# Performance work log

Measured on AMD Instinct MI355X. Metric: run time of the kernel, lower is better.

Reference implementation:

```python
import jax, jax.numpy as jnp
import numpy as np

N = 4096  # output_size
B = 4096  # batch rows
NEG_SLOPE = 0.02


def setup_inputs() -> dict:
    key = jax.random.key(0)
    k1, k2, k3, k4 = jax.random.split(key, 4)
    x = jax.random.normal(k1, (B, N), dtype=jnp.float32)
    W = jax.random.normal(k2, (N, N), dtype=jnp.float32)        # self.weights
    beta = jax.random.normal(k3, (1,), dtype=jnp.float32)       # self.beta (scalar param)
    beta_res = jax.random.normal(k4, (N,), dtype=jnp.float32)   # self.res.beta
    return {"x": x, "W": W, "beta": beta, "beta_res": beta_res}


def reference(x, W, beta, beta_res):
    # wrho = x.unsqueeze(1) * W.expand(B,-1,-1); row_sum = wrho.sum(2)  ==  x @ W.T
    row_sum = jnp.einsum("bj,ij->bi", x, W)                 # [B, N]
    out = jax.nn.relu(1.0 - beta + row_sum)                 # hlogic(1 - beta + row_sum)
    # ResEventually: relu(1 - (beta_res - (x + out))), then LeakyReLU(0.02)
    res = jax.nn.relu(1.0 - (beta_res - (x + out)))
    return jnp.where(res >= 0, res, NEG_SLOPE * res)
```

## Files before the change

### kernel.cpp

```cpp
#include <hip/hip_runtime.h>


#define NDIM 4096

typedef __bf16 bf16x8 __attribute__((ext_vector_type(8)));
typedef float f32x4 __attribute__((ext_vector_type(4)));

__device__ unsigned short f2bf(float f) {
    unsigned int x;
    __builtin_memcpy(&x, &f, 4);
    unsigned int r = x + 0x7FFFu + ((x >> 16) & 1u);
    return (unsigned short)(r >> 16);
}

__device__ unsigned int pack_bf2(float lo, float hi) {
    return (unsigned int)f2bf(lo) | ((unsigned int)f2bf(hi) << 16);
}

__device__ inline void gload16(const uint4* g, unsigned int* l) {
    __builtin_amdgcn_global_load_lds(
        (const __attribute__((address_space(1))) unsigned int*)g,
        (__attribute__((address_space(3))) unsigned int*)l,
        16, 0, 0);
}

__global__ void convert_f32_bf16_kernel(const float* X, unsigned int* Xbf,
                                        const float* W, unsigned int* Wbf) {
    unsigned int bid = blockIdx.x;
    const float* src;
    unsigned int* dst;
    if (bid < 4096) { src = X; dst = Xbf; }
    else            { src = W; dst = Wbf; bid -= 4096; }
    const size_t i = ((size_t)bid * blockDim.x + threadIdx.x) * 16;
    const f32x4* s4 = (const f32x4*)(src + i);
    f32x4 a = __builtin_nontemporal_load(s4);
    f32x4 b = __builtin_nontemporal_load(s4 + 1);
    f32x4 c = __builtin_nontemporal_load(s4 + 2);
    f32x4 d = __builtin_nontemporal_load(s4 + 3);
    uint4 u0, u1;
    u0.x = pack_bf2(a[0], a[1]);  u0.y = pack_bf2(a[2], a[3]);
    u0.z = pack_bf2(b[0], b[1]);  u0.w = pack_bf2(b[2], b[3]);
    u1.x = pack_bf2(c[0], c[1]);  u1.y = pack_bf2(c[2], c[3]);
    u1.z = pack_bf2(d[0], d[1]);  u1.w = pack_bf2(d[2], d[3]);
    uint4* o4 = (uint4*)(dst + i / 2);
    o4[0] = u0;
    o4[1] = u1;
}

#define BAR()   __builtin_amdgcn_s_barrier()
#define VMCNT(n) asm volatile("s_waitcnt vmcnt(" #n ")" ::: "memory")
#define PRIO(x) __builtin_amdgcn_s_setprio(x)

#define STAGE_A(buf, h, S) do { \
    gload16(Ab4 + (offA[2*(h)]   + (S)*8), &sAU[buf][(2*(h))*2048   + wq]); \
    gload16(Ab4 + (offA[2*(h)+1] + (S)*8), &sAU[buf][(2*(h)+1)*2048 + wq]); \
} while (0)
#define STAGE_B(buf, h, S) do { \
    gload16(Bb4 + (offB[2*(h)]   + (S)*8), &sBU[buf][(2*(h))*2048   + wq]); \
    gload16(Bb4 + (offB[2*(h)+1] + (S)*8), &sBU[buf][(2*(h)+1)*2048 + wq]); \
} while (0)

#define READ_A4(dst, pbuf, mt0) do { \
    _Pragma("unroll") for (int _m = 0; _m < 4; _m++) { \
        dst[_m][0] = (pbuf)[afB + ((mt0) + _m) * 128]; \
        dst[_m][1] = (pbuf)[afB + ((mt0) + _m) * 128 + 64]; } \
} while (0)
#define READ_B2(dst, pbuf, nt0) do { \
    _Pragma("unroll") for (int _n = 0; _n < 2; _n++) { \
        dst[_n][0] = (pbuf)[bfB + ((nt0) + _n) * 128]; \
        dst[_n][1] = (pbuf)[bfB + ((nt0) + _n) * 128 + 64]; } \
} while (0)

#define MM16(afr, bfr, mt0, nt0) do { \
    _Pragma("unroll") for (int _k = 0; _k < 2; _k++) \
    _Pragma("unroll") for (int _m = 0; _m < 4; _m++) \
    _Pragma("unroll") for (int _n = 0; _n < 2; _n++) \
        acc[(mt0)+_m][(nt0)+_n] = __builtin_amdgcn_mfma_f32_16x16x32_bf16( \
            afr[_m][_k], bfr[_n][_k], acc[(mt0)+_m][(nt0)+_n], 0, 0, 0); \
} while (0)

__global__ void __launch_bounds__(512, 2)
ResFCEventuallyLayer_82205674045459_kernel(
    const unsigned int* Xbf, const unsigned int* Wbf,
    const float* X, const float* Bp, const float* Br,
    float* out)
{
    __shared__ __align__(16) unsigned int sAU[2][8192];
    __shared__ __align__(16) unsigned int sBU[2][8192];

    const int t    = threadIdx.x;
    const int lane = t & 63;
    const int wave = t >> 6;
    const int quad = lane >> 4;
    const int l16  = lane & 15;
    const int wm   = wave >> 2;
    const int wn   = wave & 3;
    const int wq   = wave * 256;

    const int bid = blockIdx.x;
    const int swz = ((bid & 7) << 5) | (bid >> 3);
    const int bm0 = (swz >> 4) * 256;
    const int bn0 = (swz & 15) * 256;

    const uint4* Ab4 = (const uint4*)Xbf;
    const uint4* Bb4 = (const uint4*)Wbf;

    int offA[4], offB[4];
#pragma unroll
    for (int rr = 0; rr < 4; rr++) {
        const int p   = rr * 512 + t;
        const int r   = (p >> 2) & 15;
        const int sub = p >> 6;
        const int sr  = sub >> 1, sc = sub & 1;
        const int c8  = (p & 3) ^ (((r >> 3) & 1) << 1);
        const int row = sr * 16 + r;
        const int gc  = sc * 4 + c8;
        offA[rr] = (bm0 + row) * 512 + gc;
        offB[rr] = (bn0 + row) * 512 + gc;
    }

    const int laneByte = l16 * 64 + ((quad * 16) ^ (((l16 >> 3) & 1) << 5));
    const int afB = (wm * 16384 + laneByte) >> 4;
    const int bfB = (wn * 8192  + laneByte) >> 4;

    const bf16x8* pA0 = (const bf16x8*)sAU[0];
    const bf16x8* pA1 = (const bf16x8*)sAU[1];
    const bf16x8* pB0 = (const bf16x8*)sBU[0];
    const bf16x8* pB1 = (const bf16x8*)sBU[1];

    f32x4 acc[8][4];
#pragma unroll
    for (int i = 0; i < 8; i++)
#pragma unroll
        for (int j = 0; j < 4; j++)
#pragma unroll
            for (int r = 0; r < 4; r++)
                acc[i][j][r] = 0.0f;

    bf16x8 af0[4][2], af1[4][2], bf0[2][2], bf1[2][2];

    STAGE_A(0, 0, 0); STAGE_A(0, 1, 0); STAGE_B(0, 0, 0); STAGE_B(0, 1, 0);
    STAGE_B(1, 0, 1);
    STAGE_B(1, 1, 1); STAGE_A(1, 0, 1); STAGE_A(1, 1, 1);
    VMCNT(8);
    BAR();

    for (int j = 0; j < 32; j++) {
        const int S2 = (2 * j + 2) & 63;
        const int S3 = (2 * j + 3) & 63;

        READ_A4(af0, pA0, 0); READ_B2(bf0, pB0, 0); READ_B2(bf1, pB0, 2);
        PRIO(1); MM16(af0, bf0, 0, 0); MM16(af0, bf1, 0, 2); PRIO(0);
        BAR();
        STAGE_B(0, 0, S2);
        READ_A4(af1, pA0, 4);
        PRIO(1); MM16(af1, bf1, 4, 2); PRIO(0);
        BAR();
        STAGE_B(0, 1, S2); STAGE_A(0, 0, S2); STAGE_A(0, 1, S2);
        PRIO(1); MM16(af1, bf0, 4, 0); PRIO(0);
        VMCNT(8);
        BAR();

        READ_A4(af0, pA1, 0); READ_B2(bf0, pB1, 0); READ_B2(bf1, pB1, 2);
        PRIO(1); MM16(af0, bf0, 0, 0); MM16(af0, bf1, 0, 2); PRIO(0);
        BAR();
        STAGE_B(1, 0, S3);
        READ_A4(af1, pA1, 4);
        PRIO(1); MM16(af1, bf1, 4, 2); PRIO(0);
        BAR();
        STAGE_B(1, 1, S3); STAGE_A(1, 0, S3); STAGE_A(1, 1, S3);
        PRIO(1); MM16(af1, bf0, 4, 0); PRIO(0);
        VMCNT(8);
        BAR();
    }

    const float one_m_beta = 1.0f - Bp[0];
    const unsigned short* Xh = (const unsigned short*)Xbf;
#pragma unroll
    for (int nt = 0; nt < 4; nt++) {
        const int n = bn0 + wn * 64 + nt * 16 + l16;
        const float br = Br[n];
#pragma unroll
        for (int mt = 0; mt < 8; mt++) {
            const int mbase = bm0 + wm * 128 + mt * 16 + quad * 4;
#pragma unroll
            for (int r = 0; r < 4; r++) {
                const size_t idx = (size_t)(mbase + r) * NDIM + n;
                unsigned int xu = (unsigned int)Xh[idx] << 16;
                float xv;
                __builtin_memcpy(&xv, &xu, 4);
                float v = acc[mt][nt][r] + one_m_beta;
                if (v < 0.0f) v = 0.0f;
                float res = 1.0f - br + xv + v;
                if (res < 0.0f) res = 0.0f;
                __builtin_nontemporal_store(res, &out[idx]);
            }
        }
    }
    (void)X;
}

__global__ void resfc_fallback_kernel(
    const float* X, const float* W,
    const float* Bp, const float* Br,
    float* out)
{
    __shared__ __align__(16) unsigned int sA[128 * 16];
    __shared__ __align__(16) unsigned int sB[128 * 16];

    const int t    = threadIdx.x;
    const int lane = t & 63;
    const int wave = t >> 6;
    const int quad = lane >> 4;
    const int l16  = lane & 15;
    const int wm   = wave >> 1;
    const int wn   = wave & 1;

    const int bm0 = blockIdx.y * 128;
    const int bn0 = blockIdx.x * 128;

    const float* gA[4];
    const float* gB[4];
    int ldsIdx[4];
    for (int c = 0; c < 4; c++) {
        const int ch   = t + c * 256;
        const int row  = ch >> 3;
        const int col4 = ch & 7;
        gA[c] = X + (size_t)(bm0 + row) * NDIM + col4 * 4;
        gB[c] = W + (size_t)(bn0 + row) * NDIM + col4 * 4;
        ldsIdx[c] = row * 16 + col4 * 2;
    }

    const bf16x8* pa = (const bf16x8*)sA + (wm * 64 + l16) * 4 + quad;
    const bf16x8* pb = (const bf16x8*)sB + (wn * 64 + l16) * 4 + quad;

    f32x4 acc[4][4];
    for (int i = 0; i < 4; i++)
        for (int j = 0; j < 4; j++)
            for (int r = 0; r < 4; r++)
                acc[i][j][r] = 0.0f;

    for (int k0 = 0; k0 < NDIM; k0 += 32) {
        float4 va[4], vb[4];
        for (int c = 0; c < 4; c++) {
            va[c] = *(const float4*)(gA[c] + k0);
            vb[c] = *(const float4*)(gB[c] + k0);
        }
        __syncthreads();
        for (int c = 0; c < 4; c++) {
            uint2 ua, ub;
            ua.x = pack_bf2(va[c].x, va[c].y);
            ua.y = pack_bf2(va[c].z, va[c].w);
            ub.x = pack_bf2(vb[c].x, vb[c].y);
            ub.y = pack_bf2(vb[c].z, vb[c].w);
            *(uint2*)(sA + ldsIdx[c]) = ua;
            *(uint2*)(sB + ldsIdx[c]) = ub;
        }
        __syncthreads();

        bf16x8 af[4], bfr[4];
        for (int mt = 0; mt < 4; mt++) af[mt]  = pa[mt * 64];
        for (int nt = 0; nt < 4; nt++) bfr[nt] = pb[nt * 64];

        for (int mt = 0; mt < 4; mt++)
            for (int nt = 0; nt < 4; nt++)
                acc[mt][nt] = __builtin_amdgcn_mfma_f32_16x16x32_bf16(
                    af[mt], bfr[nt], acc[mt][nt], 0, 0, 0);
    }

    const float one_m_beta = 1.0f - Bp[0];
    for (int nt = 0; nt < 4; nt++) {
        const int n = bn0 + wn * 64 + nt * 16 + l16;
        const float br = Br[n];
        for (int mt = 0; mt < 4; mt++) {
            const int mbase = bm0 + wm * 64 + mt * 16 + quad * 4;
            for (int r = 0; r < 4; r++) {
                const size_t idx = (size_t)(mbase + r) * NDIM + n;
                float v = acc[mt][nt][r] + one_m_beta;
                if (v < 0.0f) v = 0.0f;
                float res = 1.0f - br + X[idx] + v;
                if (res < 0.0f) res = 0.0f;
                out[idx] = res;
            }
        }
    }
}

extern "C" void kernel_launch(void* const* d_in, const int* in_sizes, int n_in,
                              void* d_out, int out_size, void* d_ws, size_t ws_size,
                              hipStream_t stream) {
    (void)in_sizes; (void)n_in; (void)out_size;

    const float* X  = (const float*)d_in[0];
    const float* W  = (const float*)d_in[1];
    const float* Bp = (const float*)d_in[2];
    const float* Br = (const float*)d_in[3];
    float* out      = (float*)d_out;

    const size_t elems   = (size_t)NDIM * NDIM;
    const size_t bf_need = elems * 2 * 2;

    if (ws_size >= bf_need) {
        unsigned int* Xbf = (unsigned int*)d_ws;
        unsigned int* Wbf = (unsigned int*)d_ws + elems / 2;

        hipLaunchKernelGGL(convert_f32_bf16_kernel, dim3(8192), dim3(256),
                           0, stream, X, Xbf, W, Wbf);
        hipLaunchKernelGGL(ResFCEventuallyLayer_82205674045459_kernel,
                           dim3(256), dim3(512), 0, stream, Xbf, Wbf, X, Bp, Br, out);
    } else {
        hipLaunchKernelGGL(resfc_fallback_kernel,
                           dim3(NDIM / 128, NDIM / 128), dim3(256), 0, stream,
                           X, W, Bp, Br, out);
    }
}
```

Measured before the change: 297.1 us.

## Read all LDS fragments up front and cut one barrier per half-iteration

Each half-iteration of the GEMM main loop now reads all A and B fragments from LDS at the start. It then waits on lgkmcnt(0) and issues all global-to-LDS stage loads for the next K step after a single barrier, instead of splitting them around two barriers. Dropping a barrier per half-step is meant to reduce synchronisation stalls and give the MFMA chain a longer uninterrupted run. The cost is more live fragment registers and a full LDS-read wait before the prefetch. A final vmcnt(0) drains outstanding loads before the epilogue.

```diff
diff --git a/kernel.cpp b/kernel.cpp
--- a/kernel.cpp
+++ b/kernel.cpp
@@ -49,6 +49,8 @@
 
 #define BAR()   __builtin_amdgcn_s_barrier()
 #define VMCNT(n) asm volatile("s_waitcnt vmcnt(" #n ")" ::: "memory")
+#define LGKM0() do { asm volatile("s_waitcnt lgkmcnt(0)" ::: "memory"); \
+                     __builtin_amdgcn_sched_barrier(0); } while (0)
 #define PRIO(x) __builtin_amdgcn_s_setprio(x)
 
 #define STAGE_A(buf, h, S) do { \
@@ -140,8 +142,7 @@
     bf16x8 af0[4][2], af1[4][2], bf0[2][2], bf1[2][2];
 
     STAGE_A(0, 0, 0); STAGE_A(0, 1, 0); STAGE_B(0, 0, 0); STAGE_B(0, 1, 0);
-    STAGE_B(1, 0, 1);
-    STAGE_B(1, 1, 1); STAGE_A(1, 0, 1); STAGE_A(1, 1, 1);
+    STAGE_A(1, 0, 1); STAGE_A(1, 1, 1); STAGE_B(1, 0, 1); STAGE_B(1, 1, 1);
     VMCNT(8);
     BAR();
 
@@ -149,30 +150,29 @@
         const int S2 = (2 * j + 2) & 63;
         const int S3 = (2 * j + 3) & 63;
 
-        READ_A4(af0, pA0, 0); READ_B2(bf0, pB0, 0); READ_B2(bf1, pB0, 2);
+        READ_B2(bf0, pB0, 0); READ_A4(af0, pA0, 0);
+        READ_B2(bf1, pB0, 2); READ_A4(af1, pA0, 4);
         PRIO(1); MM16(af0, bf0, 0, 0); MM16(af0, bf1, 0, 2); PRIO(0);
+        LGKM0();
         BAR();
-        STAGE_B(0, 0, S2);
-        READ_A4(af1, pA0, 4);
-        PRIO(1); MM16(af1, bf1, 4, 2); PRIO(0);
-        BAR();
-        STAGE_B(0, 1, S2); STAGE_A(0, 0, S2); STAGE_A(0, 1, S2);
-        PRIO(1); MM16(af1, bf0, 4, 0); PRIO(0);
+        STAGE_B(0, 0, S2); STAGE_B(0, 1, S2);
+        STAGE_A(0, 0, S2); STAGE_A(0, 1, S2);
+        PRIO(1); MM16(af1, bf1, 4, 2); MM16(af1, bf0, 4, 0); PRIO(0);
         VMCNT(8);
         BAR();
 
-        READ_A4(af0, pA1, 0); READ_B2(bf0, pB1, 0); READ_B2(bf1, pB1, 2);
+        READ_B2(bf0, pB1, 0); READ_A4(af0, pA1, 0);
+        READ_B2(bf1, pB1, 2); READ_A4(af1, pA1, 4);
         PRIO(1); MM16(af0, bf0, 0, 0); MM16(af0, bf1, 0, 2); PRIO(0);
+        LGKM0();
         BAR();
-        STAGE_B(1, 0, S3);
-        READ_A4(af1, pA1, 4);
-        PRIO(1); MM16(af1, bf1, 4, 2); PRIO(0);
-        BAR();
-        STAGE_B(1, 1, S3); STAGE_A(1, 0, S3); STAGE_A(1, 1, S3);
-        PRIO(1); MM16(af1, bf0, 4, 0); PRIO(0);
+        STAGE_B(1, 0, S3); STAGE_B(1, 1, S3);
+        STAGE_A(1, 0, S3); STAGE_A(1, 1, S3);
+        PRIO(1); MM16(af1, bf1, 4, 2); MM16(af1, bf0, 4, 0); PRIO(0);
         VMCNT(8);
         BAR();
     }
+    VMCNT(0);
 
     const float one_m_beta = 1.0f - Bp[0];
     const unsigned short* Xh = (const unsigned short*)Xbf;
```

After: 314.9 us. 1.06x slower.
